# Kernel optimization log

Measured on AMD Instinct MI355X. Metric: run time of the kernel, lower is better.

The kernel has to match this reference:

```python
import jax, jax.numpy as jnp
import numpy as np


def setup_inputs() -> dict:
    key = jax.random.key(0)
    ks = jax.random.split(key, 6)
    B, T, C = 1, 2048, 2048
    Hq, Hkv = 32, 8
    D = C // Hq  # 64
    s = 0.02  # weight init scale for numerical stability
    return {
        "x": jax.random.normal(ks[0], (B, T, C), dtype=jnp.float32),
        "Wq": jax.random.normal(ks[1], (C, C), dtype=jnp.float32) * s,
        "Wk": jax.random.normal(ks[2], (Hkv * D, C), dtype=jnp.float32) * s,
        "Wv": jax.random.normal(ks[3], (Hkv * D, C), dtype=jnp.float32) * s,
        "Wo": jax.random.normal(ks[4], (C, C), dtype=jnp.float32) * s,
        "bo": jnp.zeros((C,), dtype=jnp.float32),
        "num_query_heads": Hq,
        "num_kv_heads": Hkv,
    }


def reference(x, Wq, Wk, Wv, Wo, bo, num_query_heads, num_kv_heads):
    B, T, C = x.shape
    Hq, Hkv = num_query_heads, num_kv_heads
    D = C // Hq
    G = Hq // Hkv  # queries per kv head

    q = (x @ Wq.T).reshape(B, T, Hkv, G, D)   # grouped query heads
    k = (x @ Wk.T).reshape(B, T, Hkv, D)
    v = (x @ Wv.T).reshape(B, T, Hkv, D)

    scale = 1.0 / jnp.sqrt(jnp.asarray(D, dtype=x.dtype))
    # [B, Hkv, G, T, T]; KV head broadcast over group dim instead of repeat_interleave
    scores = jnp.einsum("bthgd,bshd->bhgts", q, k) * scale

    causal = jnp.tril(jnp.ones((T, T), dtype=bool))  # allow j <= i
    scores = jnp.where(causal, scores, jnp.asarray(-jnp.inf, dtype=scores.dtype))
    attn = jax.nn.softmax(scores, axis=-1)  # dropout is identity at p=0.0 / eval

    out = jnp.einsum("bhgts,bshd->bthgd", attn, v).reshape(B, T, C)
    return out @ Wo.T + bo
```

## Files before the change

kernel.cpp:

```cpp
#include <hip/hip_runtime.h>
#include <hip/hip_bf16.h>

typedef __attribute__((ext_vector_type(8))) short short8;
typedef __attribute__((ext_vector_type(16))) float floatx16;
typedef __attribute__((ext_vector_type(4))) float floatx4;
typedef __attribute__((ext_vector_type(4))) unsigned uintx4;

__device__ __forceinline__ short f2bf(float f) {
    unsigned u = __builtin_bit_cast(unsigned, f);
    u += 0x7fffu + ((u >> 16) & 1u);
    return (short)(u >> 16);
}

__device__ __forceinline__ unsigned pk_bf16(float lo, float hi) {
    unsigned short a = __builtin_bit_cast(unsigned short, (__bf16)lo);
    unsigned short b = __builtin_bit_cast(unsigned short, (__bf16)hi);
    return (unsigned)a | ((unsigned)b << 16);
}

__device__ __forceinline__ void gload_lds16(const void* g, void* l) {
    __builtin_amdgcn_global_load_lds(
        (const __attribute__((address_space(1))) unsigned*)g,
        (__attribute__((address_space(3))) unsigned*)l, 16, 0, 0);
}

__global__ __launch_bounds__(256)
void convsw(const float* __restrict__ src, short* __restrict__ dst) {
    const int row = blockIdx.x;
    const int c = threadIdx.x;
    const int kt = c >> 2, cc = c & 3;
    const int cs = cc ^ ((row >> 1) & 3);
    const float* s = src + (size_t)row * 2048 + kt * 32 + cs * 8;
    float4 v0 = *(const float4*)s;
    float4 v1 = *(const float4*)(s + 4);
    short8 o = { f2bf(v0.x), f2bf(v0.y), f2bf(v0.z), f2bf(v0.w),
                 f2bf(v1.x), f2bf(v1.y), f2bf(v1.z), f2bf(v1.w) };
    *(short8*)(dst + (size_t)row * 2048 + kt * 32 + cc * 8) = o;
}

__global__ __launch_bounds__(256)
void convsw_qkv(const float* __restrict__ Wq, const float* __restrict__ Wk,
                const float* __restrict__ Wv, short* __restrict__ dst) {
    const int row = blockIdx.x;
    const float* src; int srow;
    if (row < 2048)      { src = Wq; srow = row; }
    else if (row < 2560) { src = Wk; srow = row - 2048; }
    else                 { src = Wv; srow = row - 2560; }
    const int c = threadIdx.x;
    const int kt = c >> 2, cc = c & 3;
    const int cs = cc ^ ((row >> 1) & 3);
    const float* s = src + (size_t)srow * 2048 + kt * 32 + cs * 8;
    float4 v0 = *(const float4*)s;
    float4 v1 = *(const float4*)(s + 4);
    short8 o = { f2bf(v0.x), f2bf(v0.y), f2bf(v0.z), f2bf(v0.w),
                 f2bf(v1.x), f2bf(v1.y), f2bf(v1.z), f2bf(v1.w) };
    *(short8*)(dst + (size_t)row * 2048 + kt * 32 + cc * 8) = o;
}

template<int EPI>
__global__ __launch_bounds__(256)
void gemm_sw(const short* __restrict__ A, const short* __restrict__ Bw,
             short* __restrict__ qb, short* __restrict__ kb, short* __restrict__ vt,
             float* __restrict__ fout, const float* __restrict__ bias) {
    __shared__ short As[128 * 32];
    __shared__ short Bs[128 * 32];
    constexpr int K = 2048;
    const int t = threadIdx.x, lane = t & 63, w = t >> 6;
    const int wm = w >> 1, wn = w & 1;
    const int l15 = lane & 15, lh = lane >> 4;
    const int bn = blockIdx.x, bm = blockIdx.y;
    const int ra0 = bm * 128;
    const short* Bbase = Bw + (size_t)bn * 128 * K;
    const int pr = t >> 2, pc = t & 3;

    floatx4 acc[4][4] = {};

    for (int k0 = 0; k0 < K; k0 += 32) {
        #pragma unroll
        for (int i = 0; i < 2; ++i) {
            int row = i * 64 + pr;
            gload_lds16(A + (size_t)(ra0 + row) * K + k0 + pc * 8, As + (i * 256 + t) * 8);
            gload_lds16(Bbase + (size_t)row * K + k0 + pc * 8, Bs + (i * 256 + t) * 8);
        }
        __syncthreads();
        short8 a[4], b[4];
        #pragma unroll
        for (int m = 0; m < 4; ++m) {
            int row = wm * 64 + m * 16 + l15;
            a[m] = *(const short8*)(As + row * 32 + ((lh ^ ((row >> 1) & 3)) << 3));
        }
        #pragma unroll
        for (int n = 0; n < 4; ++n) {
            int row = wn * 64 + n * 16 + l15;
            b[n] = *(const short8*)(Bs + row * 32 + ((lh ^ ((row >> 1) & 3)) << 3));
        }
        #pragma unroll
        for (int m = 0; m < 4; ++m)
            #pragma unroll
            for (int n = 0; n < 4; ++n)
                acc[m][n] = __builtin_amdgcn_mfma_f32_16x16x32_bf16(a[m], b[n], acc[m][n], 0, 0, 0);
        __syncthreads();
    }

    #pragma unroll
    for (int m = 0; m < 4; ++m) {
        #pragma unroll
        for (int n = 0; n < 4; ++n) {
            #pragma unroll
            for (int r = 0; r < 4; ++r) {
                int row = ra0 + wm * 64 + m * 16 + lh * 4 + r;
                int col = bn * 128 + wn * 64 + n * 16 + l15;
                float v = acc[m][n][r];
                if constexpr (EPI == 1) {
                    fout[(size_t)row * 2048 + col] = v + bias[col];
                } else {
                    if (col < 2048) {
                        qb[(size_t)row * 2048 + col] = f2bf(v * 0.18033688011112042f);
                    } else if (col < 2560) {
                        int kcol = col - 2048, within = kcol & 63;
                        int cp = ((within >> 3) ^ (row & 7)) & 7;
                        kb[(size_t)row * 512 + (kcol & ~63) + (cp << 3) + (within & 7)] = f2bf(v);
                    } else {
                        int dg = col - 2560;
                        int cp = (((row >> 3) & 7) ^ (dg & 7)) & 7;
                        vt[(size_t)dg * 2048 + (row & ~63) + (cp << 3) + (row & 7)] = f2bf(v);
                    }
                }
            }
        }
    }
}

__global__ __launch_bounds__(512, 4)
void attn_fwd(const short* __restrict__ qb, const short* __restrict__ kb,
              const short* __restrict__ vt, short* __restrict__ ob) {
    __shared__ __align__(16) short smem[2][16384];

    const int t = threadIdx.x, lane = t & 63, w = t >> 6;
    const int l31 = lane & 31, hi = lane >> 5;
    const int pairi = blockIdx.x;
    const int hq = blockIdx.y, hk = hq >> 2;
    const int qtA = pairi, qtB = 31 - pairi;
    const int a = w >> 1, p = w & 1;
    const int myqt = (a < 2) ? qtA : qtB;
    const int q0 = myqt * 64 + (a & 1) * 32;
    const int rg = q0 + l31;
    const int swl = l31 & 7;

    short8 qf[4];
    {
        const short* qrow = qb + (size_t)rg * 2048 + hq * 64;
        #pragma unroll
        for (int kk = 0; kk < 4; ++kk)
            qf[kk] = *(const short8*)(qrow + kk * 16 + hi * 8);
    }

    float m = -3e38f, l = 0.f;
    floatx16 acc[2] = {};

    auto stage = [&](int buf, int j0) {
        short* base = &smem[buf][0];
        #pragma unroll
        for (int i = 0; i < 4; ++i) {
            int c = i * 512 + t;
            if (i < 2) {
                int row = c >> 3, cc = c & 7;
                gload_lds16(kb + (size_t)(j0 + row) * 512 + hk * 64 + cc * 8, base + c * 8);
            } else {
                int cv = c - 1024, drow = cv >> 4, cc = cv & 15;
                gload_lds16(vt + (size_t)(hk * 64 + drow) * 2048 + j0 + cc * 8, base + c * 8);
            }
        }
    };

    const int nss = (qtB >> 1) + 1;
    stage(0, 0);
    for (int ss = 0; ss < nss; ++ss) {
        __syncthreads();
        if (ss + 1 < nss) stage((ss + 1) & 1, (ss + 1) * 128);
        const int kt = 2 * ss + p;
        if (kt <= myqt) {
            const short* K0 = &smem[ss & 1][0];
            const short* V0 = &smem[ss & 1][8192];

            floatx16 sT[2];
            #pragma unroll
            for (int kb2 = 0; kb2 < 2; ++kb2) {
                floatx16 acc2 = {};
                const int row = p * 64 + kb2 * 32 + l31;
                #pragma unroll
                for (int kk = 0; kk < 4; ++kk) {
                    short8 kf = *(const short8*)(K0 + row * 64 + (((2 * kk + hi) ^ swl) << 3));
                    acc2 = __builtin_amdgcn_mfma_f32_32x32x16_bf16(kf, qf[kk], acc2, 0, 0, 0);
                }
                sT[kb2] = acc2;
            }

            if (kt == myqt) {
                #pragma unroll
                for (int kb2 = 0; kb2 < 2; ++kb2)
                    #pragma unroll
                    for (int r = 0; r < 16; ++r) {
                        int jg = kt * 64 + kb2 * 32 + (r & 3) + 8 * (r >> 2) + 4 * hi;
                        if (jg > rg) sT[kb2][r] = -3e38f;
                    }
            }

            float v[16];
            #pragma unroll
            for (int r = 0; r < 16; ++r) v[r] = fmaxf(sT[0][r], sT[1][r]);
            #pragma unroll
            for (int st = 8; st >= 1; st >>= 1)
                #pragma unroll
                for (int r = 0; r < 8; ++r)
                    if (r < st) v[r] = fmaxf(v[r], v[r + st]);
            float tm = fmaxf(v[0], __shfl_xor(v[0], 32));

            if (!__all(tm <= m + 8.0f)) {
                float mn = fmaxf(m, tm);
                float sf = __builtin_amdgcn_exp2f(m - mn);
                m = mn;
                l *= sf;
                #pragma unroll
                for (int n = 0; n < 2; ++n)
                    #pragma unroll
                    for (int r = 0; r < 16; ++r) acc[n][r] *= sf;
            }

            float sv[16];
            #pragma unroll
            for (int kb2 = 0; kb2 < 2; ++kb2)
                #pragma unroll
                for (int r = 0; r < 16; ++r)
                    sT[kb2][r] = __builtin_amdgcn_exp2f(sT[kb2][r] - m);
            #pragma unroll
            for (int r = 0; r < 16; ++r) sv[r] = sT[0][r] + sT[1][r];
            #pragma unroll
            for (int st = 8; st >= 1; st >>= 1)
                #pragma unroll
                for (int r = 0; r < 8; ++r)
                    if (r < st) sv[r] += sv[r + st];
            l += sv[0] + __shfl_xor(sv[0], 32);

            #pragma unroll
            for (int kb2 = 0; kb2 < 2; ++kb2) {
                unsigned Qd[8], Pd[8];
                #pragma unroll
                for (int c = 0; c < 8; ++c)
                    Qd[c] = pk_bf16(sT[kb2][2 * c], sT[kb2][2 * c + 1]);
                #pragma unroll
                for (int c = 0; c < 8; ++c)
                    Pd[c] = __shfl_xor(Qd[c], 32);
                #pragma unroll
                for (int b = 0; b < 2; ++b) {
                    uintx4 j;
                    if (b == 0) {
                        j.x = hi ? Pd[2] : Qd[0];
                        j.y = hi ? Pd[3] : Qd[1];
                        j.z = hi ? Qd[2] : Pd[0];
                        j.w = hi ? Qd[3] : Pd[1];
                    } else {
                        j.x = hi ? Pd[6] : Qd[4];
                        j.y = hi ? Pd[7] : Qd[5];
                        j.z = hi ? Qd[6] : Pd[4];
                        j.w = hi ? Qd[7] : Pd[5];
                    }
                    short8 pf = __builtin_bit_cast(short8, j);
                    const int kk = kb2 * 2 + b;
                    const int ch = p * 64 + (((2 * kk + hi) ^ swl) << 3);
                    short8 vf0 = *(const short8*)(V0 + l31 * 128 + ch);
                    acc[0] = __builtin_amdgcn_mfma_f32_32x32x16_bf16(vf0, pf, acc[0], 0, 0, 0);
                    short8 vf1 = *(const short8*)(V0 + (32 + l31) * 128 + ch);
                    acc[1] = __builtin_amdgcn_mfma_f32_32x32x16_bf16(vf1, pf, acc[1], 0, 0, 0);
                }
            }
        }
    }

    __syncthreads();
    float* mb = (float*)&smem[0][0] + ((size_t)a * 64 + lane) * 34;
    if (p == 1) {
        #pragma unroll
        for (int n = 0; n < 2; ++n)
            #pragma unroll
            for (int r = 0; r < 16; ++r) mb[n * 16 + r] = acc[n][r];
        mb[32] = m;
        mb[33] = l;
    }
    __syncthreads();
    if (p == 0) {
        const float m1 = mb[32], l1 = mb[33];
        const float M = fmaxf(m, m1);
        const float sf0 = __builtin_amdgcn_exp2f(m - M);
        const float sf1 = __builtin_amdgcn_exp2f(m1 - M);
        const float linv = 1.0f / (sf0 * l + sf1 * l1);
        const int sw = (rg >> 1) & 3;
        #pragma unroll
        for (int n = 0; n < 2; ++n) {
            #pragma unroll
            for (int g = 0; g < 4; ++g) {
                #pragma unroll
                for (int e = 0; e < 4; e += 2) {
                    int r = 4 * g + e;
                    float o0 = (sf0 * acc[n][r]     + sf1 * mb[n * 16 + r])     * linv;
                    float o1 = (sf0 * acc[n][r + 1] + sf1 * mb[n * 16 + r + 1]) * linv;
                    unsigned pkv = pk_bf16(o0, o1);
                    int d = 32 * n + e + 8 * g + 4 * hi;
                    int col = hq * 64 + d;
                    int cp = ((col >> 3) & 3) ^ sw;
                    *(unsigned*)(ob + (size_t)rg * 2048 + (col & ~31) + (cp << 3) + (col & 7)) = pkv;
                }
            }
        }
    }
}

extern "C" void kernel_launch(void* const* d_in, const int* in_sizes, int n_in,
                              void* d_out, int out_size, void* d_ws, size_t ws_size,
                              hipStream_t stream) {
    const float* x  = (const float*)d_in[0];
    const float* Wq = (const float*)d_in[1];
    const float* Wk = (const float*)d_in[2];
    const float* Wv = (const float*)d_in[3];
    const float* Wo = (const float*)d_in[4];
    const float* bo = (const float*)d_in[5];

    char* ws = (char*)d_ws;
    short* xb   = (short*)ws;
    short* wqkv = (short*)(ws + ((size_t)8  << 20));
    short* qb   = (short*)(ws + ((size_t)20 << 20));
    short* kb   = (short*)(ws + ((size_t)28 << 20));
    short* vt   = (short*)(ws + ((size_t)30 << 20));
    short* ob   = xb;
    short* wob  = wqkv;

    convsw<<<2048, 256, 0, stream>>>(x, xb);
    convsw_qkv<<<3072, 256, 0, stream>>>(Wq, Wk, Wv, wqkv);
    gemm_sw<0><<<dim3(24, 16), 256, 0, stream>>>(xb, wqkv, qb, kb, vt, nullptr, nullptr);
    convsw<<<2048, 256, 0, stream>>>(Wo, wob);
    attn_fwd<<<dim3(16, 32), 512, 0, stream>>>(qb, kb, vt, ob);
    gemm_sw<1><<<dim3(16, 16), 256, 0, stream>>>(ob, wob, nullptr, nullptr, nullptr,
                                                 (float*)d_out, bo);
}
```

Before: 147.1 us.

## Double-buffer GEMM with 64-wide K tiles, 8 waves, and merged conversion kernels

Rewrites the projection GEMMs to use 512-thread blocks with double-buffered LDS staging of 64-wide K tiles. The next tile's global-to-LDS load is issued before computing the current one, so the load overlaps the MFMA work and one barrier per iteration is removed. The 8-way XOR swizzle replaces the old 4-way one, and the attention output writer and the conversion kernels are updated to match the new layout. The x and Wqkv conversions are merged into one launch, and the output projection uses a narrower 64-column tile to launch more blocks. The trade-off is higher LDS use per block, which may limit occupancy.

```diff
diff --git a/kernel.cpp b/kernel.cpp
--- a/kernel.cpp
+++ b/kernel.cpp
@@ -28,88 +28,111 @@
 void convsw(const float* __restrict__ src, short* __restrict__ dst) {
     const int row = blockIdx.x;
     const int c = threadIdx.x;
-    const int kt = c >> 2, cc = c & 3;
-    const int cs = cc ^ ((row >> 1) & 3);
-    const float* s = src + (size_t)row * 2048 + kt * 32 + cs * 8;
+    const int kt = c >> 3, cc = c & 7;
+    const float* s = src + (size_t)row * 2048 + kt * 64 + (cc ^ (row & 7)) * 8;
     float4 v0 = *(const float4*)s;
     float4 v1 = *(const float4*)(s + 4);
     short8 o = { f2bf(v0.x), f2bf(v0.y), f2bf(v0.z), f2bf(v0.w),
                  f2bf(v1.x), f2bf(v1.y), f2bf(v1.z), f2bf(v1.w) };
-    *(short8*)(dst + (size_t)row * 2048 + kt * 32 + cc * 8) = o;
+    *(short8*)(dst + (size_t)row * 2048 + kt * 64 + cc * 8) = o;
 }
 
 __global__ __launch_bounds__(256)
-void convsw_qkv(const float* __restrict__ Wq, const float* __restrict__ Wk,
-                const float* __restrict__ Wv, short* __restrict__ dst) {
-    const int row = blockIdx.x;
-    const float* src; int srow;
-    if (row < 2048)      { src = Wq; srow = row; }
-    else if (row < 2560) { src = Wk; srow = row - 2048; }
-    else                 { src = Wv; srow = row - 2560; }
+void conv_all(const float* __restrict__ x, const float* __restrict__ Wq,
+              const float* __restrict__ Wk, const float* __restrict__ Wv,
+              short* __restrict__ xb, short* __restrict__ wqkv) {
+    const int bid = blockIdx.x;
+    const float* src; short* dst; int srow, drow;
+    if (bid < 2048)      { src = x;  dst = xb;   srow = bid;        drow = bid; }
+    else {
+        int r = bid - 2048;
+        dst = wqkv; drow = r;
+        if (r < 2048)      { src = Wq; srow = r; }
+        else if (r < 2560) { src = Wk; srow = r - 2048; }
+        else               { src = Wv; srow = r - 2560; }
+    }
     const int c = threadIdx.x;
-    const int kt = c >> 2, cc = c & 3;
-    const int cs = cc ^ ((row >> 1) & 3);
-    const float* s = src + (size_t)srow * 2048 + kt * 32 + cs * 8;
+    const int kt = c >> 3, cc = c & 7;
+    const float* s = src + (size_t)srow * 2048 + kt * 64 + (cc ^ (drow & 7)) * 8;
     float4 v0 = *(const float4*)s;
     float4 v1 = *(const float4*)(s + 4);
     short8 o = { f2bf(v0.x), f2bf(v0.y), f2bf(v0.z), f2bf(v0.w),
                  f2bf(v1.x), f2bf(v1.y), f2bf(v1.z), f2bf(v1.w) };
-    *(short8*)(dst + (size_t)row * 2048 + kt * 32 + cc * 8) = o;
-}
-
-template<int EPI>
-__global__ __launch_bounds__(256)
-void gemm_sw(const short* __restrict__ A, const short* __restrict__ Bw,
-             short* __restrict__ qb, short* __restrict__ kb, short* __restrict__ vt,
-             float* __restrict__ fout, const float* __restrict__ bias) {
-    __shared__ short As[128 * 32];
-    __shared__ short Bs[128 * 32];
+    *(short8*)(dst + (size_t)drow * 2048 + kt * 64 + cc * 8) = o;
+}
+
+template<int BN, int EPI>
+__global__ __launch_bounds__(512, 4)
+void gemm8(const short* __restrict__ A, const short* __restrict__ Bw,
+           short* __restrict__ qb, short* __restrict__ kb, short* __restrict__ vt,
+           float* __restrict__ fout, const float* __restrict__ bias) {
     constexpr int K = 2048;
+    constexpr int NN = BN / 32;
+    constexpr int ACH = 128 * 8;
+    constexpr int NCH = (128 + BN) * 8;
+    __shared__ short sm[2][(128 + BN) * 64];
+
     const int t = threadIdx.x, lane = t & 63, w = t >> 6;
-    const int wm = w >> 1, wn = w & 1;
+    const int wm = w & 3, wn = w >> 2;
     const int l15 = lane & 15, lh = lane >> 4;
     const int bn = blockIdx.x, bm = blockIdx.y;
     const int ra0 = bm * 128;
-    const short* Bbase = Bw + (size_t)bn * 128 * K;
-    const int pr = t >> 2, pc = t & 3;
-
-    floatx4 acc[4][4] = {};
-
-    for (int k0 = 0; k0 < K; k0 += 32) {
-        #pragma unroll
-        for (int i = 0; i < 2; ++i) {
-            int row = i * 64 + pr;
-            gload_lds16(A + (size_t)(ra0 + row) * K + k0 + pc * 8, As + (i * 256 + t) * 8);
-            gload_lds16(Bbase + (size_t)row * K + k0 + pc * 8, Bs + (i * 256 + t) * 8);
-        }
+    const short* Bbase = Bw + (size_t)bn * BN * K;
+
+    floatx4 acc[2][NN] = {};
+
+    auto stage = [&](int buf, int k0) {
+        short* base = &sm[buf][0];
+        #pragma unroll
+        for (int i = 0; i < NCH / 512; ++i) {
+            int c = i * 512 + t;
+            if (c < ACH) {
+                int row = c >> 3, cc = c & 7;
+                gload_lds16(A + (size_t)(ra0 + row) * K + k0 + cc * 8, base + c * 8);
+            } else {
+                int c2 = c - ACH;
+                int row = c2 >> 3, cc = c2 & 7;
+                gload_lds16(Bbase + (size_t)row * K + k0 + cc * 8, base + (ACH + c2) * 8);
+            }
+        }
+    };
+
+    stage(0, 0);
+    #pragma unroll 1
+    for (int it = 0; it < K / 64; ++it) {
         __syncthreads();
-        short8 a[4], b[4];
-        #pragma unroll
-        for (int m = 0; m < 4; ++m) {
-            int row = wm * 64 + m * 16 + l15;
-            a[m] = *(const short8*)(As + row * 32 + ((lh ^ ((row >> 1) & 3)) << 3));
-        }
-        #pragma unroll
-        for (int n = 0; n < 4; ++n) {
-            int row = wn * 64 + n * 16 + l15;
-            b[n] = *(const short8*)(Bs + row * 32 + ((lh ^ ((row >> 1) & 3)) << 3));
-        }
-        #pragma unroll
-        for (int m = 0; m < 4; ++m)
-            #pragma unroll
-            for (int n = 0; n < 4; ++n)
-                acc[m][n] = __builtin_amdgcn_mfma_f32_16x16x32_bf16(a[m], b[n], acc[m][n], 0, 0, 0);
-        __syncthreads();
+        if (it + 1 < K / 64) stage((it + 1) & 1, (it + 1) * 64);
+        const short* As = &sm[it & 1][0];
+        const short* Bs = As + 128 * 64;
+        #pragma unroll
+        for (int kf = 0; kf < 2; ++kf) {
+            short8 a[2], b[NN];
+            #pragma unroll
+            for (int m = 0; m < 2; ++m) {
+                int arow = wm * 32 + m * 16 + l15;
+                a[m] = *(const short8*)(As + arow * 64 + (((kf * 4 + lh) ^ (arow & 7)) << 3));
+            }
+            #pragma unroll
+            for (int n = 0; n < NN; ++n) {
+                int brow = wn * (BN / 2) + n * 16 + l15;
+                b[n] = *(const short8*)(Bs + brow * 64 + (((kf * 4 + lh) ^ (brow & 7)) << 3));
+            }
+            #pragma unroll
+            for (int m = 0; m < 2; ++m)
+                #pragma unroll
+                for (int n = 0; n < NN; ++n)
+                    acc[m][n] = __builtin_amdgcn_mfma_f32_16x16x32_bf16(a[m], b[n], acc[m][n], 0, 0, 0);
+        }
     }
 
     #pragma unroll
-    for (int m = 0; m < 4; ++m) {
-        #pragma unroll
-        for (int n = 0; n < 4; ++n) {
+    for (int m = 0; m < 2; ++m) {
+        #pragma unroll
+        for (int n = 0; n < NN; ++n) {
             #pragma unroll
             for (int r = 0; r < 4; ++r) {
-                int row = ra0 + wm * 64 + m * 16 + lh * 4 + r;
-                int col = bn * 128 + wn * 64 + n * 16 + l15;
+                int row = ra0 + wm * 32 + m * 16 + lh * 4 + r;
+                int col = bn * BN + wn * (BN / 2) + n * 16 + l15;
                 float v = acc[m][n][r];
                 if constexpr (EPI == 1) {
                     fout[(size_t)row * 2048 + col] = v + bias[col];
@@ -294,7 +317,7 @@
         const float sf0 = __builtin_amdgcn_exp2f(m - M);
         const float sf1 = __builtin_amdgcn_exp2f(m1 - M);
         const float linv = 1.0f / (sf0 * l + sf1 * l1);
-        const int sw = (rg >> 1) & 3;
+        const int sw8 = rg & 7;
         #pragma unroll
         for (int n = 0; n < 2; ++n) {
             #pragma unroll
@@ -307,8 +330,8 @@
                     unsigned pkv = pk_bf16(o0, o1);
                     int d = 32 * n + e + 8 * g + 4 * hi;
                     int col = hq * 64 + d;
-                    int cp = ((col >> 3) & 3) ^ sw;
-                    *(unsigned*)(ob + (size_t)rg * 2048 + (col & ~31) + (cp << 3) + (col & 7)) = pkv;
+                    int cp = ((col >> 3) & 7) ^ sw8;
+                    *(unsigned*)(ob + (size_t)rg * 2048 + (col & ~63) + (cp << 3) + (col & 7)) = pkv;
                 }
             }
         }
@@ -334,11 +357,10 @@
     short* ob   = xb;
     short* wob  = wqkv;
 
-    convsw<<<2048, 256, 0, stream>>>(x, xb);
-    convsw_qkv<<<3072, 256, 0, stream>>>(Wq, Wk, Wv, wqkv);
-    gemm_sw<0><<<dim3(24, 16), 256, 0, stream>>>(xb, wqkv, qb, kb, vt, nullptr, nullptr);
+    conv_all<<<5120, 256, 0, stream>>>(x, Wq, Wk, Wv, xb, wqkv);
+    gemm8<128, 0><<<dim3(24, 16), 512, 0, stream>>>(xb, wqkv, qb, kb, vt, nullptr, nullptr);
     convsw<<<2048, 256, 0, stream>>>(Wo, wob);
     attn_fwd<<<dim3(16, 32), 512, 0, stream>>>(qb, kb, vt, ob);
-    gemm_sw<1><<<dim3(16, 16), 256, 0, stream>>>(ob, wob, nullptr, nullptr, nullptr,
-                                                 (float*)d_out, bo);
-}
+    gemm8<64, 1><<<dim3(32, 16), 512, 0, stream>>>(ob, wob, nullptr, nullptr, nullptr,
+                                                   (float*)d_out, bo);
+}
```

New measurement: 122.4 us. 1.2x faster.
